# Optimization experiments

Measured on AMD Instinct MI355X. Metric: run time of the kernel, lower is better.

The kernel has to match this reference:

```python
import jax, jax.numpy as jnp
import numpy as np

N = 200      # nodes (fixed by Linear(200,100) on x.T)
E = 8000     # edges
NFEAT, NHID, NCLASS = 8192, 2048, 512


def _cheb_conv(x, edge_index, edge_weight, W, b):
    """PyG ChebConv (K=3, sym norm, lambda_max=2): L_hat = -D^{-1/2} A D^{-1/2}.
    T0 = x, T1 = L_hat x, T2 = 2 L_hat T1 - T0; out = sum_k T_k @ W[k] + b."""
    row, col = edge_index[0], edge_index[1]
    deg = jax.ops.segment_sum(edge_weight, row, num_segments=N)
    safe = jnp.where(deg > 0, deg, 1.0)
    dinv = jnp.where(deg > 0, 1.0 / jnp.sqrt(safe), 0.0)
    norm = -dinv[row] * edge_weight * dinv[col]  # [E]

    def lap(z):  # messages from source j=row to target i=col
        return jax.ops.segment_sum(norm[:, None] * z[row], col, num_segments=N)

    T1 = lap(x)
    T2 = 2.0 * lap(T1) - x
    return x @ W[0] + T1 @ W[1] + T2 @ W[2] + b


def _forward_single(x, ei, ew, W1, b1, W2, b2):
    h = jax.nn.relu(_cheb_conv(x, ei, ew, W1, b1))
    # dropout is identity in eval mode
    return _cheb_conv(h, ei, ew, W2, b2)  # [N, NCLASS]


def _classifier(z, Wc1, bc1, Wc2, bc2, Wc3, bc3):
    h = jax.nn.relu(z @ Wc1.T + bc1)
    h = jax.nn.relu(h @ Wc2.T + bc2)
    return h @ Wc3.T + bc3  # [NCLASS, 1]


def setup_inputs() -> dict:
    key = jax.random.key(0)
    ks = jax.random.split(key, 12)
    inp = {
        'x1': jax.random.normal(ks[0], (N, NFEAT), jnp.float32),
        'edge_index1': jax.random.randint(ks[1], (2, E), 0, N, jnp.int64),
        'edge_attr1': jax.random.uniform(ks[2], (E,), jnp.float32),
        'x2': jax.random.normal(ks[3], (N, NFEAT), jnp.float32),
        'edge_index2': jax.random.randint(ks[4], (2, E), 0, N, jnp.int64),
        'edge_attr2': jax.random.uniform(ks[5], (E,), jnp.float32),
        'W1': jax.random.normal(ks[6], (3, NFEAT, NHID), jnp.float32) * (NFEAT ** -0.5),
        'b1': jnp.zeros((NHID,), jnp.float32),
        'W2': jax.random.normal(ks[7], (3, NHID, NCLASS), jnp.float32) * (NHID ** -0.5),
        'b2': jnp.zeros((NCLASS,), jnp.float32),
        'Wc1': jax.random.normal(ks[8], (100, 200), jnp.float32) * (200 ** -0.5),
        'bc1': jnp.zeros((100,), jnp.float32),
        'Wc2': jax.random.normal(ks[9], (50, 100), jnp.float32) * (100 ** -0.5),
        'bc2': jnp.zeros((50,), jnp.float32),
        'Wc3': jax.random.normal(ks[10], (1, 50), jnp.float32) * (50 ** -0.5),
        'bc3': jnp.zeros((1,), jnp.float32),
    }
    return inp


def reference(x1, edge_index1, edge_attr1, x2, edge_index2, edge_attr2,
              W1, b1, W2, b2, Wc1, bc1, Wc2, bc2, Wc3, bc3):
    o1 = _forward_single(x1, edge_index1, edge_attr1, W1, b1, W2, b2)
    o2 = _forward_single(x2, edge_index2, edge_attr2, W1, b1, W2, b2)
    out1 = _classifier(o1.T, Wc1, bc1, Wc2, bc2, Wc3, bc3)  # [NCLASS, 1]
    out2 = _classifier(o2.T, Wc1, bc1, Wc2, bc2, Wc3, bc3)
    return out1, out2
```

## Files before the change

### kernel.cpp

```cpp
#include <hip/hip_runtime.h>

typedef __attribute__((ext_vector_type(8))) short short8;
typedef __attribute__((ext_vector_type(4))) float f32x4;
typedef __attribute__((ext_vector_type(2))) float f32x2;
typedef __attribute__((ext_vector_type(4))) unsigned int u32x4;

#define NNODES 200
#define NEDGE  8000
#define NF1    8192
#define NH     2048
#define NCL    512
#define K1     24576
#define K2     6144
#define MR     512
#define MV     400
#define PV     400
#define KC1    16
#define BK1    1536
#define KC2    16
#define BK2    384

#define OFF_P1  0ull
#define SZ_P1   (16ull*PV*NH*4)
#define OFF_P2  (OFF_P1 + SZ_P1)
#define SZ_P2   (16ull*PV*NCL*4)
#define OFF_A1  (OFF_P2 + SZ_P2)
#define SZ_A1   ((unsigned long long)MR*K1*2)
#define OFF_A2  (OFF_A1 + SZ_A1)
#define SZ_A2   ((unsigned long long)MR*K2*2)
#define OFF_DEG (OFF_A2 + SZ_A2)
#define OFF_LD  (OFF_DEG + 2048)
#define OFF_LL  (OFF_LD + 320000ull)
#define OFF_Z   OFF_P1

static __device__ __forceinline__ unsigned short f2bf(float f) {
  unsigned int u = __float_as_uint(f);
  unsigned int r = (u + 0x7fffu + ((u >> 16) & 1u)) >> 16;
  return (unsigned short)r;
}
static __device__ __forceinline__ unsigned packbf(float a, float b) {
  return (unsigned)f2bf(a) | ((unsigned)f2bf(b) << 16);
}

__global__ void k_zero(f32x4* p1, int n1, f32x4* p2, int n2, f32x4* p3, int n3) {
  int i = blockIdx.x * 256 + threadIdx.x;
  f32x4 z = {0.f, 0.f, 0.f, 0.f};
  if (i < n1) p1[i] = z;
  i -= n1;
  if (i >= 0 && i < n2) p2[i] = z;
  i -= n2;
  if (i >= 0 && i < n3) p3[i] = z;
}

__global__ void k_deg(const int* __restrict__ ei1, const float* __restrict__ ew1,
                      const int* __restrict__ ei2, const float* __restrict__ ew2,
                      float* __restrict__ deg) {
  int e = blockIdx.x * 256 + threadIdx.x;
  if (e >= 2 * NEDGE) return;
  int g = e / NEDGE, k = e % NEDGE;
  const int* ei = g ? ei2 : ei1;
  const float* ew = g ? ew2 : ew1;
  atomicAdd(deg + g * NNODES + ei[k], ew[k]);
}

__global__ void k_buildL(const int* __restrict__ ei1, const float* __restrict__ ew1,
                         const int* __restrict__ ei2, const float* __restrict__ ew2,
                         const float* __restrict__ deg, float* __restrict__ Ld) {
  int e = blockIdx.x * 256 + threadIdx.x;
  if (e >= 2 * NEDGE) return;
  int g = e / NEDGE, k = e % NEDGE;
  const int* ei = g ? ei2 : ei1;
  const float* ew = g ? ew2 : ew1;
  int r = ei[k], c = ei[NEDGE + k];
  float dr = deg[g * NNODES + r], dc = deg[g * NNODES + c];
  float ir = dr > 0.f ? 1.0f / sqrtf(dr) : 0.f;
  float ic = dc > 0.f ? 1.0f / sqrtf(dc) : 0.f;
  float nrm = -ir * ew[k] * ic;
  atomicAdd(Ld + ((size_t)g * NNODES + c) * NNODES + r, nrm);
}

__global__ void k_LL(const float* __restrict__ Ld, unsigned short* __restrict__ LLb) {
  int b = blockIdx.x;
  int g = b / NNODES, i = b % NNODES;
  __shared__ float Lr[NNODES];
  const float* Lg = Ld + (size_t)g * NNODES * NNODES;
  int t = threadIdx.x;
  if (t < NNODES) Lr[t] = Lg[i * NNODES + t];
  __syncthreads();
  if (t < NNODES) {
    float acc = 0.f;
    for (int k = 0; k < NNODES; ++k) acc = fmaf(Lr[k], Lg[k * NNODES + t], acc);
    unsigned short* LLg = LLb + (size_t)g * MR * 224;
    LLg[(size_t)i * 224 + t] = f2bf(Lr[t]);
    LLg[(size_t)(NNODES + i) * 224 + t] = f2bf(2.f * acc - (i == t ? 1.f : 0.f));
  }
}

__global__ void k_t0(const float* __restrict__ x1, const float* __restrict__ x2,
                     unsigned short* __restrict__ A1) {
  int gid = blockIdx.x * 256 + threadIdx.x;
  int row = gid / (NF1 / 8);
  int c8 = (gid % (NF1 / 8)) * 8;
  const float* xp = (row < NNODES ? x1 + (size_t)row * NF1
                                  : x2 + (size_t)(row - NNODES) * NF1) + c8;
  f32x4 a = *(const f32x4*)xp;
  f32x4 b = *(const f32x4*)(xp + 4);
  u32x4 o;
  o[0] = packbf(a[0], a[1]);
  o[1] = packbf(a[2], a[3]);
  o[2] = packbf(b[0], b[1]);
  o[3] = packbf(b[2], b[3]);
  *(u32x4*)(A1 + (size_t)row * K1 + c8) = o;
}

__global__ __launch_bounds__(256, 1)
void k_abuild(const unsigned short* __restrict__ LLb, const unsigned short* __restrict__ Asrc,
              unsigned short* __restrict__ Adst, const int Nf, const int Ka) {
  __shared__ __align__(16) unsigned short XF[7][4][64][8];
  const int g = blockIdx.x & 1;
  const int nt = blockIdx.x >> 1;
  const int nbase = nt * 64;
  const int t = threadIdx.x;

  #pragma unroll
  for (int it = 0; it < 14; ++it) {
    const int pos = it * 256 + t;
    const int j = pos >> 4;
    const int n4 = (pos & 15) * 4;
    unsigned long long v = 0ull;
    if (j < NNODES)
      v = *(const unsigned long long*)(Asrc + (size_t)(g * NNODES + j) * Ka + nbase + n4);
    const int ks = j >> 5, kg = (j >> 3) & 3, jj = j & 7;
    #pragma unroll
    for (int e = 0; e < 4; ++e) {
      const int nn = n4 + e;
      XF[ks][nn >> 4][(nn & 15) + 16 * kg][jj] = (unsigned short)(v >> (16 * e));
    }
  }
  __syncthreads();

  const int w = t >> 6, lane = t & 63;
  const int lm = lane & 15, lk8 = (lane >> 4) * 8;
  f32x4 acc[7][4];
  #pragma unroll
  for (int i = 0; i < 7; ++i)
    #pragma unroll
    for (int j = 0; j < 4; ++j) acc[i][j] = (f32x4){0.f, 0.f, 0.f, 0.f};

  const unsigned short* LLg = LLb + (size_t)g * MR * 224;
  #pragma unroll
  for (int ks = 0; ks < 7; ++ks) {
    short8 bfr[4];
    #pragma unroll
    for (int nf = 0; nf < 4; ++nf) bfr[nf] = *(const short8*)&XF[ks][nf][lane][0];
    short8 af[7];
    #pragma unroll
    for (int mf = 0; mf < 7; ++mf)
      af[mf] = *(const short8*)(LLg + (size_t)(w * 112 + mf * 16 + lm) * 224 + ks * 32 + lk8);
    #pragma unroll
    for (int mf = 0; mf < 7; ++mf)
      #pragma unroll
      for (int nf = 0; nf < 4; ++nf)
        acc[mf][nf] = __builtin_amdgcn_mfma_f32_16x16x32_bf16(af[mf], bfr[nf], acc[mf][nf], 0, 0, 0);
  }

  const int lr4 = (lane >> 4) * 4;
  #pragma unroll
  for (int mf = 0; mf < 7; ++mf) {
    #pragma unroll
    for (int ri = 0; ri < 4; ++ri) {
      const int m = w * 112 + mf * 16 + lr4 + ri;
      if (m < MV) {
        const int drow = g * NNODES + (m < NNODES ? m : m - NNODES);
        const size_t dbase = (size_t)drow * Ka + (m < NNODES ? Nf : 2 * Nf) + nbase + lm;
        #pragma unroll
        for (int nf = 0; nf < 4; ++nf)
          Adst[dbase + nf * 16] = f2bf(acc[mf][nf][ri]);
      }
    }
  }
}

template <int BN, int KA>
__global__ __launch_bounds__(512, 4)
void k_gemm(const float* __restrict__ W, const unsigned short* __restrict__ A,
            float* __restrict__ P, const int Nn, const int BK) {
  constexpr int NF = BN / 16;
  constexpr int NFW = BN / 32;
  constexpr int CW = BN / 16;
  __shared__ __align__(16) unsigned short Atile[MR * 64];
  __shared__ __align__(16) unsigned short Wt[2 * NF * 64 * 8];

  const int t = threadIdx.x;
  const int w = t >> 6, lane = t & 63;
  const int wm = w >> 1, wn = w & 1;
  const int lm = lane & 15;
  const int l4 = lane >> 4;
  const int kc = blockIdx.x & 15;
  const int nt = blockIdx.x >> 4;
  const int kbase = kc * BK;
  const int nbase = nt * BN;
  const int nks = BK >> 6;

  const int arow0 = t >> 3;
  const int agb = ((t * 16) & 127) ^ ((arow0 & 7) << 4);
  const char* Ab = (const char*)A + (size_t)kbase * 2 + (size_t)arow0 * (KA * 2) + agb;
  const size_t CSTEP = (size_t)64 * KA * 2;

  const int kk0 = (t >> 4) * 2;
  const int colb = (t & 15) * CW;
  const float* Wg = W + (size_t)(kbase + kk0) * Nn + nbase + colb;
  int offWl[CW];
  {
    const int ks = kk0 >> 5, kg = (kk0 >> 3) & 3, jj1 = (kk0 & 7) >> 1;
    #pragma unroll
    for (int e = 0; e < CW; ++e) {
      const int nn = colb + e;
      const int nf = nn >> 4;
      const int ln = ((nn & 15) + 16 * kg) ^ (nf & 3);
      offWl[e] = ((ks * NF + nf) * 64 + ln) * 4 + jj1;
    }
  }

  const int aBase = (wm * 128 + lm) * 128 + ((l4 * 16) ^ ((lm & 7) << 4));
  int bAddr[NFW];
  #pragma unroll
  for (int nf = 0; nf < NFW; ++nf) {
    const int nfg = wn * NFW + nf;
    bAddr[nf] = ((nfg * 64) + (lane ^ (nfg & 3))) * 16;
  }
  constexpr int BSTRIDE = NF * 64 * 16;

  f32x4 acc[8][NFW];
  #pragma unroll
  for (int i = 0; i < 8; ++i)
    #pragma unroll
    for (int j = 0; j < NFW; ++j) acc[i][j] = (f32x4){0.f, 0.f, 0.f, 0.f};

  u32x4 areg[7];
  f32x4 w0_4, w1_4;
  f32x2 w0_2, w1_2;

  auto loadW = [&](int kt) {
    const float* p = Wg + (size_t)kt * 64 * Nn;
    if constexpr (BN == 64) {
      w0_4 = __builtin_nontemporal_load((const f32x4*)p);
      w1_4 = __builtin_nontemporal_load((const f32x4*)(p + Nn));
    } else {
      w0_2 = __builtin_nontemporal_load((const f32x2*)p);
      w1_2 = __builtin_nontemporal_load((const f32x2*)(p + Nn));
    }
  };
  auto storeW = [&]() {
    unsigned* w32 = (unsigned*)Wt;
    #pragma unroll
    for (int e = 0; e < CW; ++e) {
      if constexpr (BN == 64) w32[offWl[e]] = packbf(w0_4[e], w1_4[e]);
      else                    w32[offWl[e]] = packbf(w0_2[e], w1_2[e]);
    }
  };

  #pragma unroll
  for (int c = 0; c < 8; ++c) {
    u32x4 v = *(const u32x4*)(Ab + c * CSTEP);
    *(u32x4*)((char*)Atile + c * 8192 + t * 16) = v;
  }
  loadW(0);
  storeW();
  __syncthreads();

  for (int kt = 0; kt < nks; ++kt) {
    const bool more = (kt + 1 < nks);
    if (more) loadW(kt + 1);
    #pragma unroll
    for (int ks = 0; ks < 2; ++ks) {
      short8 bfr[NFW];
      #pragma unroll
      for (int nf = 0; nf < NFW; ++nf)
        bfr[nf] = *(const short8*)((const char*)Wt + bAddr[nf] + ks * BSTRIDE);
      const int abx = aBase ^ (ks * 64);
      short8 af[8];
      #pragma unroll
      for (int mf = 0; mf < 8; ++mf)
        af[mf] = *(const short8*)((const char*)Atile + abx + mf * 2048);
      #pragma unroll
      for (int mf = 0; mf < 8; ++mf)
        #pragma unroll
        for (int nf = 0; nf < NFW; ++nf)
          acc[mf][nf] = __builtin_amdgcn_mfma_f32_16x16x32_bf16(af[mf], bfr[nf], acc[mf][nf], 0, 0, 0);
    }
    if (more) {
      #pragma unroll
      for (int c = 0; c < 7; ++c)
        areg[c] = *(const u32x4*)(Ab + c * CSTEP + (size_t)(kt + 1) * 128);
    }
    __syncthreads();
    if (more) {
      #pragma unroll
      for (int c = 0; c < 7; ++c)
        *(u32x4*)((char*)Atile + c * 8192 + t * 16) = areg[c];
      storeW();
    }
    __syncthreads();
  }

  float* Pk = P + ((size_t)kc * PV) * Nn + nbase;
  #pragma unroll
  for (int mf = 0; mf < 8; ++mf) {
    const int row0 = wm * 128 + mf * 16 + l4 * 4;
    #pragma unroll
    for (int ri = 0; ri < 4; ++ri) {
      const int row = row0 + ri;
      if (row < MV) {
        #pragma unroll
        for (int nf = 0; nf < NFW; ++nf) {
          const int col = (wn * NFW + nf) * 16 + lm;
          __builtin_nontemporal_store(acc[mf][nf][ri], Pk + (size_t)row * Nn + col);
        }
      }
    }
  }
}

__global__ void k_ep1(const float* __restrict__ P1, const float* __restrict__ b1,
                      unsigned short* __restrict__ A2) {
  int gid = blockIdx.x * 256 + threadIdx.x;
  int row = gid / (NH / 4);
  int c = (gid % (NH / 4)) * 4;
  f32x4 s = {0.f, 0.f, 0.f, 0.f};
  #pragma unroll
  for (int kc = 0; kc < KC1; ++kc)
    s += __builtin_nontemporal_load((const f32x4*)(P1 + ((size_t)kc * PV + row) * NH + c));
  const f32x4 b = *(const f32x4*)(b1 + c);
  unsigned long long pack = 0;
  #pragma unroll
  for (int i = 0; i < 4; ++i) {
    float v = s[i] + b[i];
    pack |= (unsigned long long)f2bf(v > 0.f ? v : 0.f) << (16 * i);
  }
  *(unsigned long long*)(A2 + (size_t)row * K2 + c) = pack;
}

__global__ __launch_bounds__(256)
void k_zsum(const float* __restrict__ P2, const float* __restrict__ b2,
            float* __restrict__ zt) {
  __shared__ float tile[8][520];
  const int g = blockIdx.x / 25;
  const int j0 = (blockIdx.x % 25) * 8;
  const int t = threadIdx.x;
  const int j = t >> 5;
  const int c0 = (t & 31) * 16;
  const int row = g * NNODES + j0 + j;

  #pragma unroll
  for (int ci = 0; ci < 4; ++ci) {
    const int c = c0 + ci * 4;
    f32x4 s = *(const f32x4*)(b2 + c);
    #pragma unroll
    for (int kc = 0; kc < KC2; ++kc)
      s += __builtin_nontemporal_load((const f32x4*)(P2 + ((size_t)kc * PV + row) * NCL + c));
    *(f32x4*)&tile[j][c] = s;
  }
  __syncthreads();

  #pragma unroll
  for (int ci = 0; ci < 2; ++ci) {
    const int c = ci * 256 + t;
    f32x4 lo, hi;
    #pragma unroll
    for (int e = 0; e < 4; ++e) { lo[e] = tile[e][c]; hi[e] = tile[4 + e][c]; }
    float* zr = zt + ((size_t)g * NCL + c) * 200 + j0;
    *(f32x4*)zr = lo;
    *(f32x4*)(zr + 4) = hi;
  }
}

__global__ __launch_bounds__(256)
void k_cls2(const float* __restrict__ zt,
            const float* __restrict__ Wc1, const float* __restrict__ bc1,
            const float* __restrict__ Wc2, const float* __restrict__ bc2,
            const float* __restrict__ Wc3, const float* __restrict__ bc3,
            float* __restrict__ outp) {
  __shared__ float zs[4][200];
  __shared__ float h1s[4][100];
  __shared__ float h2s[4][50];
  const int g = blockIdx.x >> 7;
  const int t = threadIdx.x;
  const int w = t >> 6, lane = t & 63;
  const int r = (blockIdx.x & 127) * 4 + w;

  const float* zr = zt + ((size_t)g * NCL + r) * 200;
  #pragma unroll
  for (int i = 0; i < 4; ++i) {
    const int idx = i * 64 + lane;
    if (idx < 200) zs[w][idx] = zr[idx];
  }
  __syncthreads();

  {
    const int c0 = lane;
    const int c1 = lane + 64;
    const int c1m = (c1 < 100) ? c1 : 99;
    float a0 = bc1[c0 < 100 ? c0 : 99];
    float a1 = bc1[c1m];
    const float* w0 = Wc1 + c0 * 200;
    const float* w1 = Wc1 + c1m * 200;
    #pragma unroll 8
    for (int j = 0; j < 200; ++j) {
      const float zv = zs[w][j];
      a0 = fmaf(zv, w0[j], a0);
      a1 = fmaf(zv, w1[j], a1);
    }
    if (c0 < 100) h1s[w][c0] = a0 > 0.f ? a0 : 0.f;
    if (c1 < 100) h1s[w][c1] = a1 > 0.f ? a1 : 0.f;
  }
  __syncthreads();

  {
    const int c2 = (lane < 50) ? lane : 49;
    float b = bc2[c2];
    const float* w2 = Wc2 + c2 * 100;
    #pragma unroll 10
    for (int c = 0; c < 100; ++c) b = fmaf(h1s[w][c], w2[c], b);
    if (lane < 50) h2s[w][lane] = b > 0.f ? b : 0.f;
  }
  __syncthreads();

  {
    float v = (lane < 50) ? h2s[w][lane] * Wc3[lane] : 0.f;
    #pragma unroll
    for (int off = 32; off >= 1; off >>= 1) v += __shfl_down(v, off);
    if (lane == 0) outp[g * NCL + r] = v + bc3[0];
  }
}

extern "C" void kernel_launch(void* const* d_in, const int* in_sizes, int n_in,
                              void* d_out, int out_size, void* d_ws, size_t ws_size,
                              hipStream_t stream) {
  const float* x1  = (const float*)d_in[0];
  const int*   ei1 = (const int*)d_in[1];
  const float* ea1 = (const float*)d_in[2];
  const float* x2  = (const float*)d_in[3];
  const int*   ei2 = (const int*)d_in[4];
  const float* ea2 = (const float*)d_in[5];
  const float* W1  = (const float*)d_in[6];
  const float* b1  = (const float*)d_in[7];
  const float* W2  = (const float*)d_in[8];
  const float* b2  = (const float*)d_in[9];
  const float* Wc1 = (const float*)d_in[10];
  const float* bc1 = (const float*)d_in[11];
  const float* Wc2 = (const float*)d_in[12];
  const float* bc2 = (const float*)d_in[13];
  const float* Wc3 = (const float*)d_in[14];
  const float* bc3 = (const float*)d_in[15];
  float* outp = (float*)d_out;

  char* ws = (char*)d_ws;
  float*          P1  = (float*)(ws + OFF_P1);
  float*          P2  = (float*)(ws + OFF_P2);
  unsigned short* A1  = (unsigned short*)(ws + OFF_A1);
  unsigned short* A2  = (unsigned short*)(ws + OFF_A2);
  float*          deg = (float*)(ws + OFF_DEG);
  float*          Ld  = (float*)(ws + OFF_LD);
  unsigned short* LLb = (unsigned short*)(ws + OFF_LL);
  float*          zt  = (float*)(ws + OFF_Z);

  k_zero<<<1871, 256, 0, stream>>>(
      (f32x4*)(ws + OFF_DEG), 48800,
      (f32x4*)(ws + OFF_A1 + (size_t)MV * K1 * 2), 344064,
      (f32x4*)(ws + OFF_A2 + (size_t)MV * K2 * 2), 86016);

  k_deg<<<63, 256, 0, stream>>>(ei1, ea1, ei2, ea2, deg);
  k_buildL<<<63, 256, 0, stream>>>(ei1, ea1, ei2, ea2, deg, Ld);
  k_LL<<<400, 256, 0, stream>>>(Ld, LLb);
  k_t0<<<1600, 256, 0, stream>>>(x1, x2, A1);
  k_abuild<<<(NF1 / 64) * 2, 256, 0, stream>>>(LLb, A1, A1, NF1, K1);
  k_gemm<64, K1><<<KC1 * (NH / 64), 512, 0, stream>>>(W1, A1, P1, NH, BK1);
  k_ep1<<<800, 256, 0, stream>>>(P1, b1, A2);
  k_abuild<<<(NH / 64) * 2, 256, 0, stream>>>(LLb, A2, A2, NH, K2);
  k_gemm<32, K2><<<KC2 * (NCL / 32), 512, 0, stream>>>(W2, A2, P2, NCL, BK2);
  k_zsum<<<50, 256, 0, stream>>>(P2, b2, zt);
  k_cls2<<<256, 256, 0, stream>>>(zt, Wc1, bc1, Wc2, bc2, Wc3, bc3, outp);
}
```

Measured before the change: 214.2 us.

## Double-buffer GEMM LDS tiles, widen layer-1 N tile, trim padded rows, split zsum

The GEMM kernel now keeps two LDS buffers for both the A and W tiles. This removes one barrier per k-step and issues the next A loads in the middle of the MFMA loop. The padded A row count drops from 512 to 448, so each wave covers 112 rows, which shrinks the zeroing kernel and the LDS footprint. The first-layer GEMM uses 128-column tiles, which halves the number of times the A operand is re-read, and occupancy is lowered to 2 blocks per CU to fit the doubled LDS. The zsum kernel is also split across twice as many blocks.

```diff
diff --git a/kernel.cpp b/kernel.cpp
--- a/kernel.cpp
+++ b/kernel.cpp
@@ -12,7 +12,7 @@
 #define NCL    512
 #define K1     24576
 #define K2     6144
-#define MR     512
+#define MR     448
 #define MV     400
 #define PV     400
 #define KC1    16
@@ -182,14 +182,17 @@
 }
 
 template <int BN, int KA>
-__global__ __launch_bounds__(512, 4)
+__global__ __launch_bounds__(512, 2)
 void k_gemm(const float* __restrict__ W, const unsigned short* __restrict__ A,
             float* __restrict__ P, const int Nn, const int BK) {
   constexpr int NF = BN / 16;
   constexpr int NFW = BN / 32;
   constexpr int CW = BN / 16;
-  __shared__ __align__(16) unsigned short Atile[MR * 64];
-  __shared__ __align__(16) unsigned short Wt[2 * NF * 64 * 8];
+  constexpr int ABUF = MR * 128;
+  constexpr int BSTRIDE = NF * 1024;
+  constexpr int WBUF = 2 * BSTRIDE;
+  __shared__ __align__(16) unsigned short Atile[2 * MR * 64];
+  __shared__ __align__(16) unsigned short Wt[2 * NF * 1024];
 
   const int t = threadIdx.x;
   const int w = t >> 6, lane = t & 63;
@@ -212,102 +215,113 @@
   const float* Wg = W + (size_t)(kbase + kk0) * Nn + nbase + colb;
   int offWl[CW];
   {
-    const int ks = kk0 >> 5, kg = (kk0 >> 3) & 3, jj1 = (kk0 & 7) >> 1;
+    const int ks0 = kk0 >> 5, kg0 = (kk0 >> 3) & 3, jj1 = (kk0 & 7) >> 1;
     #pragma unroll
     for (int e = 0; e < CW; ++e) {
       const int nn = colb + e;
       const int nf = nn >> 4;
-      const int ln = ((nn & 15) + 16 * kg) ^ (nf & 3);
-      offWl[e] = ((ks * NF + nf) * 64 + ln) * 4 + jj1;
-    }
-  }
-
-  const int aBase = (wm * 128 + lm) * 128 + ((l4 * 16) ^ ((lm & 7) << 4));
+      const int ln = ((nn & 15) + 16 * kg0) ^ (nf & 3);
+      offWl[e] = ((ks0 * NF + nf) * 64 + ln) * 4 + jj1;
+    }
+  }
+
+  const int aBase = (wm * 112 + lm) * 128 + ((l4 * 16) ^ ((lm & 7) << 4));
   int bAddr[NFW];
   #pragma unroll
   for (int nf = 0; nf < NFW; ++nf) {
     const int nfg = wn * NFW + nf;
-    bAddr[nf] = ((nfg * 64) + (lane ^ (nfg & 3))) * 16;
-  }
-  constexpr int BSTRIDE = NF * 64 * 16;
-
-  f32x4 acc[8][NFW];
-  #pragma unroll
-  for (int i = 0; i < 8; ++i)
+    bAddr[nf] = nfg * 1024 + (lane ^ (nfg & 3)) * 16;
+  }
+
+  f32x4 acc[7][NFW];
+  #pragma unroll
+  for (int i = 0; i < 7; ++i)
     #pragma unroll
     for (int j = 0; j < NFW; ++j) acc[i][j] = (f32x4){0.f, 0.f, 0.f, 0.f};
 
   u32x4 areg[7];
-  f32x4 w0_4, w1_4;
-  f32x2 w0_2, w1_2;
+  f32x4 w0a, w0b, w1a, w1b;
+  f32x2 w0s, w1s;
 
   auto loadW = [&](int kt) {
     const float* p = Wg + (size_t)kt * 64 * Nn;
-    if constexpr (BN == 64) {
-      w0_4 = __builtin_nontemporal_load((const f32x4*)p);
-      w1_4 = __builtin_nontemporal_load((const f32x4*)(p + Nn));
+    if constexpr (BN == 128) {
+      w0a = __builtin_nontemporal_load((const f32x4*)p);
+      w0b = __builtin_nontemporal_load((const f32x4*)(p + 4));
+      w1a = __builtin_nontemporal_load((const f32x4*)(p + Nn));
+      w1b = __builtin_nontemporal_load((const f32x4*)(p + Nn + 4));
     } else {
-      w0_2 = __builtin_nontemporal_load((const f32x2*)p);
-      w1_2 = __builtin_nontemporal_load((const f32x2*)(p + Nn));
+      w0s = __builtin_nontemporal_load((const f32x2*)p);
+      w1s = __builtin_nontemporal_load((const f32x2*)(p + Nn));
     }
   };
-  auto storeW = [&]() {
-    unsigned* w32 = (unsigned*)Wt;
+  auto loadA = [&](int kt) {
+    #pragma unroll
+    for (int c = 0; c < 7; ++c)
+      areg[c] = *(const u32x4*)(Ab + c * CSTEP + (size_t)kt * 128);
+  };
+  auto storeA = [&](int buf) {
+    #pragma unroll
+    for (int c = 0; c < 7; ++c)
+      *(u32x4*)((char*)Atile + buf * ABUF + c * 8192 + t * 16) = areg[c];
+  };
+  auto storeW = [&](int buf) {
+    unsigned* w32 = (unsigned*)Wt + buf * (WBUF / 4);
     #pragma unroll
     for (int e = 0; e < CW; ++e) {
-      if constexpr (BN == 64) w32[offWl[e]] = packbf(w0_4[e], w1_4[e]);
-      else                    w32[offWl[e]] = packbf(w0_2[e], w1_2[e]);
+      float lo, hi;
+      if constexpr (BN == 128) {
+        lo = (e < 4) ? w0a[e & 3] : w0b[e & 3];
+        hi = (e < 4) ? w1a[e & 3] : w1b[e & 3];
+      } else {
+        lo = w0s[e & 1];
+        hi = w1s[e & 1];
+      }
+      w32[offWl[e]] = packbf(lo, hi);
     }
   };
 
-  #pragma unroll
-  for (int c = 0; c < 8; ++c) {
-    u32x4 v = *(const u32x4*)(Ab + c * CSTEP);
-    *(u32x4*)((char*)Atile + c * 8192 + t * 16) = v;
-  }
   loadW(0);
-  storeW();
+  loadA(0);
+  storeA(0);
+  storeW(0);
   __syncthreads();
 
   for (int kt = 0; kt < nks; ++kt) {
+    const int buf = kt & 1;
     const bool more = (kt + 1 < nks);
     if (more) loadW(kt + 1);
+
     #pragma unroll
     for (int ks = 0; ks < 2; ++ks) {
       short8 bfr[NFW];
       #pragma unroll
       for (int nf = 0; nf < NFW; ++nf)
-        bfr[nf] = *(const short8*)((const char*)Wt + bAddr[nf] + ks * BSTRIDE);
-      const int abx = aBase ^ (ks * 64);
-      short8 af[8];
+        bfr[nf] = *(const short8*)((const char*)Wt + buf * WBUF + bAddr[nf] + ks * BSTRIDE);
+      const int abx = (aBase ^ (ks * 64)) + buf * ABUF;
+      short8 af[7];
       #pragma unroll
-      for (int mf = 0; mf < 8; ++mf)
+      for (int mf = 0; mf < 7; ++mf)
         af[mf] = *(const short8*)((const char*)Atile + abx + mf * 2048);
       #pragma unroll
-      for (int mf = 0; mf < 8; ++mf)
+      for (int mf = 0; mf < 7; ++mf)
         #pragma unroll
         for (int nf = 0; nf < NFW; ++nf)
           acc[mf][nf] = __builtin_amdgcn_mfma_f32_16x16x32_bf16(af[mf], bfr[nf], acc[mf][nf], 0, 0, 0);
-    }
+      if (ks == 0 && more) loadA(kt + 1);
+    }
+
     if (more) {
-      #pragma unroll
-      for (int c = 0; c < 7; ++c)
-        areg[c] = *(const u32x4*)(Ab + c * CSTEP + (size_t)(kt + 1) * 128);
+      storeA(buf ^ 1);
+      storeW(buf ^ 1);
     }
     __syncthreads();
-    if (more) {
-      #pragma unroll
-      for (int c = 0; c < 7; ++c)
-        *(u32x4*)((char*)Atile + c * 8192 + t * 16) = areg[c];
-      storeW();
-    }
-    __syncthreads();
   }
 
   float* Pk = P + ((size_t)kc * PV) * Nn + nbase;
   #pragma unroll
-  for (int mf = 0; mf < 8; ++mf) {
-    const int row0 = wm * 128 + mf * 16 + l4 * 4;
+  for (int mf = 0; mf < 7; ++mf) {
+    const int row0 = wm * 112 + mf * 16 + l4 * 4;
     #pragma unroll
     for (int ri = 0; ri < 4; ++ri) {
       const int row = row0 + ri;
@@ -344,35 +358,34 @@
 __global__ __launch_bounds__(256)
 void k_zsum(const float* __restrict__ P2, const float* __restrict__ b2,
             float* __restrict__ zt) {
-  __shared__ float tile[8][520];
-  const int g = blockIdx.x / 25;
-  const int j0 = (blockIdx.x % 25) * 8;
+  __shared__ float tile[8][264];
+  const int b = blockIdx.x;
+  const int g = b / 50;
+  const int r2 = b % 50;
+  const int j0 = (r2 >> 1) * 8;
+  const int ch = (r2 & 1) * 256;
   const int t = threadIdx.x;
   const int j = t >> 5;
-  const int c0 = (t & 31) * 16;
+  const int c0 = (t & 31) * 8;
   const int row = g * NNODES + j0 + j;
 
   #pragma unroll
-  for (int ci = 0; ci < 4; ++ci) {
+  for (int ci = 0; ci < 2; ++ci) {
     const int c = c0 + ci * 4;
-    f32x4 s = *(const f32x4*)(b2 + c);
+    f32x4 s = *(const f32x4*)(b2 + ch + c);
     #pragma unroll
     for (int kc = 0; kc < KC2; ++kc)
-      s += __builtin_nontemporal_load((const f32x4*)(P2 + ((size_t)kc * PV + row) * NCL + c));
+      s += __builtin_nontemporal_load((const f32x4*)(P2 + ((size_t)kc * PV + row) * NCL + ch + c));
     *(f32x4*)&tile[j][c] = s;
   }
   __syncthreads();
 
-  #pragma unroll
-  for (int ci = 0; ci < 2; ++ci) {
-    const int c = ci * 256 + t;
-    f32x4 lo, hi;
-    #pragma unroll
-    for (int e = 0; e < 4; ++e) { lo[e] = tile[e][c]; hi[e] = tile[4 + e][c]; }
-    float* zr = zt + ((size_t)g * NCL + c) * 200 + j0;
-    *(f32x4*)zr = lo;
-    *(f32x4*)(zr + 4) = hi;
-  }
+  f32x4 lo, hi;
+  #pragma unroll
+  for (int e = 0; e < 4; ++e) { lo[e] = tile[e][t]; hi[e] = tile[4 + e][t]; }
+  float* zr = zt + ((size_t)g * NCL + ch + t) * 200 + j0;
+  *(f32x4*)zr = lo;
+  *(f32x4*)(zr + 4) = hi;
 }
 
 __global__ __launch_bounds__(256)
@@ -465,20 +478,20 @@
   unsigned short* LLb = (unsigned short*)(ws + OFF_LL);
   float*          zt  = (float*)(ws + OFF_Z);
 
-  k_zero<<<1871, 256, 0, stream>>>(
-      (f32x4*)(ws + OFF_DEG), 48800,
-      (f32x4*)(ws + OFF_A1 + (size_t)MV * K1 * 2), 344064,
-      (f32x4*)(ws + OFF_A2 + (size_t)MV * K2 * 2), 86016);
+  k_zero<<<897, 256, 0, stream>>>(
+      (f32x4*)(ws + OFF_DEG), 45216,
+      (f32x4*)(ws + OFF_A1 + (size_t)MV * K1 * 2), 147456,
+      (f32x4*)(ws + OFF_A2 + (size_t)MV * K2 * 2), 36864);
 
   k_deg<<<63, 256, 0, stream>>>(ei1, ea1, ei2, ea2, deg);
   k_buildL<<<63, 256, 0, stream>>>(ei1, ea1, ei2, ea2, deg, Ld);
   k_LL<<<400, 256, 0, stream>>>(Ld, LLb);
   k_t0<<<1600, 256, 0, stream>>>(x1, x2, A1);
   k_abuild<<<(NF1 / 64) * 2, 256, 0, stream>>>(LLb, A1, A1, NF1, K1);
-  k_gemm<64, K1><<<KC1 * (NH / 64), 512, 0, stream>>>(W1, A1, P1, NH, BK1);
+  k_gemm<128, K1><<<KC1 * (NH / 128), 512, 0, stream>>>(W1, A1, P1, NH, BK1);
   k_ep1<<<800, 256, 0, stream>>>(P1, b1, A2);
   k_abuild<<<(NH / 64) * 2, 256, 0, stream>>>(LLb, A2, A2, NH, K2);
   k_gemm<32, K2><<<KC2 * (NCL / 32), 512, 0, stream>>>(W2, A2, P2, NCL, BK2);
-  k_zsum<<<50, 256, 0, stream>>>(P2, b2, zt);
+  k_zsum<<<100, 256, 0, stream>>>(P2, b2, zt);
   k_cls2<<<256, 256, 0, stream>>>(zt, Wc1, bc1, Wc2, bc2, Wc3, bc3, outp);
 }
```

Measured after the change: 177.0 us. -17.3%, faster.
